# Kernel tuning notes

Hardware: AMD Instinct MI355X
Metric: run time of the kernel (lower is better)

Reference implementation:

```python
import jax, jax.numpy as jnp
import numpy as np

DIN = 4096
DOUT = 12288
NUM_GATES = DOUT // 3
OFFSET = 1
BS = 4096
Z = 1.0

# fixed 3x5 combine matrix from the module
M = jnp.array([[1., 0., 0., 0., 0.],
               [0., 0., 1., 1., -1.],
               [0., 1., 0., -1., 1.]], dtype=jnp.float32)


def _make_connections():
    g = np.arange(NUM_GATES, dtype=np.int64)
    starts = (g * 3 + OFFSET) % DIN
    conn = (starts[:, None] + np.arange(3, dtype=np.int64)[None, :]) % DIN
    return jnp.asarray(conn, dtype=jnp.int32)


def setup_inputs() -> dict:
    key = jax.random.key(0)
    kx, kw = jax.random.split(key)
    x = jax.random.normal(kx, (BS, DIN), dtype=jnp.float32)
    wgts = jax.random.normal(kw, (NUM_GATES, 3, 4), dtype=jnp.float32)
    connections = _make_connections()
    return {"x": x, "wgts": wgts, "connections": connections}


def reference(x, wgts, connections):
    bs = x.shape[0]
    # gather 3 inputs per gate: [bs, G, 3]
    gathered = x[:, connections]
    # append constant z -> [bs, G, 4]
    zcol = jnp.full((bs, NUM_GATES, 1), Z, dtype=x.dtype)
    inp = jnp.concatenate([gathered, zcol], axis=-1)
    # softmax-weighted small matmul (training path): [G,3,4] x [bs,G,4] -> [bs,G,3]
    wp = jax.nn.softmax(wgts, axis=-1)
    s = jnp.einsum('gik,bgk->bgi', wp, inp)
    # elementwise products -> [bs, G, 5]
    v4 = s[..., 0] * s[..., 1]
    v5 = s[..., 0] * s[..., 2]
    feats = jnp.concatenate([s, v4[..., None], v5[..., None]], axis=-1)
    # fixed 3x5 combine: [bs, G, 3]
    signals = jnp.einsum('rk,bgk->bgr', M, feats)
    # strided slice ::3 on last dim (size 3) keeps only index 0 -> [bs, G]
    out = signals[:, :, ::3].reshape(bs, -1)
    return out
```

## Files before the change

kernel.cpp:

```cpp
#include <hip/hip_runtime.h>

#define DIN 4096
#define NG  4096
#define BS  4096
#define RPB 8
#define BT  1024

typedef float v4f __attribute__((ext_vector_type(4)));

__global__ __launch_bounds__(BT, 4) void fredkin_s0_stream(
    const float* __restrict__ x,
    const float* __restrict__ wgts,
    float* __restrict__ out)
{
    const int tid = threadIdx.x;
    const int l   = tid & 63;
    const int g0  = 4 * tid;

    float4 wq[4];
#pragma unroll
    for (int j = 0; j < 4; ++j) {
        float4 r = *reinterpret_cast<const float4*>(wgts + (size_t)(g0 + j) * 12);
        float m  = fmaxf(fmaxf(r.x, r.y), fmaxf(r.z, r.w));
        float e0 = __expf(r.x - m);
        float e1 = __expf(r.y - m);
        float e2 = __expf(r.z - m);
        float e3 = __expf(r.w - m);
        float inv = 1.0f / (e0 + e1 + e2 + e3);
        wq[j] = make_float4(e0 * inv, e1 * inv, e2 * inv, e3 * inv);
    }

    const int brow = blockIdx.x * RPB;
    const float* xb   = x   + (size_t)brow * DIN;
    float*       orow = out + (size_t)brow * NG + g0;

    const int lb = (12 * tid) & (DIN - 1);
    const int i1 = (lb + 4)  & (DIN - 1);
    const int i2 = (lb + 8)  & (DIN - 1);
    const int i3 = (lb + 12) & (DIN - 1);

#pragma unroll
    for (int r = 0; r < RPB; ++r) {
        const float* xr = xb + (size_t)r * DIN;
        float4 f0 = *reinterpret_cast<const float4*>(xr + lb);
        float4 f1 = *reinterpret_cast<const float4*>(xr + i1);
        float4 f2 = *reinterpret_cast<const float4*>(xr + i2);
        float e12 = __shfl_down(f0.x, 1);
        if (l == 63) e12 = xr[i3];
        v4f o;
        o.x = fmaf(wq[0].x, f0.y, fmaf(wq[0].y, f0.z, fmaf(wq[0].z, f0.w, wq[0].w)));
        o.y = fmaf(wq[1].x, f1.x, fmaf(wq[1].y, f1.y, fmaf(wq[1].z, f1.z, wq[1].w)));
        o.z = fmaf(wq[2].x, f1.w, fmaf(wq[2].y, f2.x, fmaf(wq[2].z, f2.y, wq[2].w)));
        o.w = fmaf(wq[3].x, f2.z, fmaf(wq[3].y, f2.w, fmaf(wq[3].z, e12, wq[3].w)));
        __builtin_nontemporal_store(o, reinterpret_cast<v4f*>(orow + (size_t)r * NG));
    }
}

extern "C" void kernel_launch(void* const* d_in, const int* in_sizes, int n_in,
                              void* d_out, int out_size, void* d_ws, size_t ws_size,
                              hipStream_t stream) {
    const float* x    = (const float*)d_in[0];
    const float* wgts = (const float*)d_in[1];
    float* out = (float*)d_out;

    fredkin_s0_stream<<<dim3(BS / RPB), dim3(BT), 0, stream>>>(x, wgts, out);
}
```

Measured before the change: 127.2 us.

## Stage input rows through LDS ring buffer with async global-to-LDS loads

Replaces direct per-thread float4 global loads of x with a 4-buffer LDS ring filled by global_load_lds DMA, prefetching up to three rows ahead, with manual vmcnt waits and a barrier per row. Gates are remapped so each thread handles gates tid+1024k, which gives coalesced scalar output stores in place of per-thread float4 stores, and reads of the gathered inputs come from LDS. The aim is to overlap row loads with compute and stores and to avoid the shuffle and edge-case scalar load. In exchange it adds 16 KB of LDS per block, a barrier on every row, and fragile hand-counted waitcnt values that mix in the store counts.

```diff
diff --git a/kernel.cpp b/kernel.cpp
--- a/kernel.cpp
+++ b/kernel.cpp
@@ -1,59 +1,100 @@
 #include <hip/hip_runtime.h>
 
-#define DIN 4096
-#define NG  4096
-#define BS  4096
-#define RPB 8
-#define BT  1024
+#define DIN  4096
+#define NG   4096
+#define BS   4096
+#define RPB  8
+#define BT   1024
 
-typedef float v4f __attribute__((ext_vector_type(4)));
+#define WAITVM(N) __builtin_amdgcn_s_waitcnt((N) | 0x0F70)
 
-__global__ __launch_bounds__(BT, 4) void fredkin_s0_stream(
+__device__ __forceinline__ void dma16(const float* g, float* lds) {
+    __builtin_amdgcn_global_load_lds(
+        (const __attribute__((address_space(1))) void*)g,
+        (__attribute__((address_space(3))) void*)lds, 16, 0, 0);
+}
+
+__global__ __launch_bounds__(BT, 8) void fredkin_ring4(
     const float* __restrict__ x,
     const float* __restrict__ wgts,
     float* __restrict__ out)
 {
+    __shared__ float B0[DIN], B1[DIN], B2[DIN], B3[DIN];
+
     const int tid = threadIdx.x;
+    const int w   = tid >> 6;
     const int l   = tid & 63;
-    const int g0  = 4 * tid;
 
     float4 wq[4];
 #pragma unroll
-    for (int j = 0; j < 4; ++j) {
-        float4 r = *reinterpret_cast<const float4*>(wgts + (size_t)(g0 + j) * 12);
+    for (int k = 0; k < 4; ++k) {
+        const int g = tid + (k << 10);
+        float4 r = *reinterpret_cast<const float4*>(wgts + (size_t)g * 12);
         float m  = fmaxf(fmaxf(r.x, r.y), fmaxf(r.z, r.w));
         float e0 = __expf(r.x - m);
         float e1 = __expf(r.y - m);
         float e2 = __expf(r.z - m);
         float e3 = __expf(r.w - m);
         float inv = 1.0f / (e0 + e1 + e2 + e3);
-        wq[j] = make_float4(e0 * inv, e1 * inv, e2 * inv, e3 * inv);
+        wq[k] = make_float4(e0 * inv, e1 * inv, e2 * inv, e3 * inv);
     }
 
     const int brow = blockIdx.x * RPB;
     const float* xb   = x   + (size_t)brow * DIN;
-    float*       orow = out + (size_t)brow * NG + g0;
+    float*       obase = out + (size_t)brow * NG + tid;
+    const int doff = (w << 8) + (l << 2);
 
-    const int lb = (12 * tid) & (DIN - 1);
-    const int i1 = (lb + 4)  & (DIN - 1);
-    const int i2 = (lb + 8)  & (DIN - 1);
-    const int i3 = (lb + 12) & (DIN - 1);
+    int idx[4][3];
+#pragma unroll
+    for (int k = 0; k < 4; ++k) {
+        const int jb = 3 * tid + 3072 * k;
+#pragma unroll
+        for (int j = 0; j < 3; ++j) idx[k][j] = (jb + 1 + j) & (DIN - 1);
+    }
 
-#pragma unroll
-    for (int r = 0; r < RPB; ++r) {
-        const float* xr = xb + (size_t)r * DIN;
-        float4 f0 = *reinterpret_cast<const float4*>(xr + lb);
-        float4 f1 = *reinterpret_cast<const float4*>(xr + i1);
-        float4 f2 = *reinterpret_cast<const float4*>(xr + i2);
-        float e12 = __shfl_down(f0.x, 1);
-        if (l == 63) e12 = xr[i3];
-        v4f o;
-        o.x = fmaf(wq[0].x, f0.y, fmaf(wq[0].y, f0.z, fmaf(wq[0].z, f0.w, wq[0].w)));
-        o.y = fmaf(wq[1].x, f1.x, fmaf(wq[1].y, f1.y, fmaf(wq[1].z, f1.z, wq[1].w)));
-        o.z = fmaf(wq[2].x, f1.w, fmaf(wq[2].y, f2.x, fmaf(wq[2].z, f2.y, wq[2].w)));
-        o.w = fmaf(wq[3].x, f2.z, fmaf(wq[3].y, f2.w, fmaf(wq[3].z, e12, wq[3].w)));
-        __builtin_nontemporal_store(o, reinterpret_cast<v4f*>(orow + (size_t)r * NG));
+#define STAGE(BUF, R_) dma16(xb + (size_t)(R_) * DIN + doff, (BUF) + (w << 8));
+
+    asm volatile("" ::: "memory");
+    STAGE(B0, 0)
+    STAGE(B1, 1)
+    STAGE(B2, 2)
+
+#define FRED_ITER(R_, NWAIT, RBUF, WBUF, DO_STAGE)                            \
+    {                                                                         \
+        asm volatile("" ::: "memory");                                        \
+        WAITVM(NWAIT);                               \
+        __builtin_amdgcn_s_barrier();      \
+        asm volatile("" ::: "memory");                                        \
+        if (DO_STAGE) STAGE(WBUF, (R_) + 3)                                   \
+        float* orow = obase + (size_t)(R_) * NG;                              \
+        float o0 = fmaf(wq[0].x, RBUF[idx[0][0]],                             \
+                   fmaf(wq[0].y, RBUF[idx[0][1]],                             \
+                   fmaf(wq[0].z, RBUF[idx[0][2]], wq[0].w)));                 \
+        float o1 = fmaf(wq[1].x, RBUF[idx[1][0]],                             \
+                   fmaf(wq[1].y, RBUF[idx[1][1]],                             \
+                   fmaf(wq[1].z, RBUF[idx[1][2]], wq[1].w)));                 \
+        float o2 = fmaf(wq[2].x, RBUF[idx[2][0]],                             \
+                   fmaf(wq[2].y, RBUF[idx[2][1]],                             \
+                   fmaf(wq[2].z, RBUF[idx[2][2]], wq[2].w)));                 \
+        float o3 = fmaf(wq[3].x, RBUF[idx[3][0]],                             \
+                   fmaf(wq[3].y, RBUF[idx[3][1]],                             \
+                   fmaf(wq[3].z, RBUF[idx[3][2]], wq[3].w)));                 \
+        __builtin_nontemporal_store(o0, orow);                                \
+        __builtin_nontemporal_store(o1, orow + 1024);                         \
+        __builtin_nontemporal_store(o2, orow + 2048);                         \
+        __builtin_nontemporal_store(o3, orow + 3072);                         \
     }
+
+    FRED_ITER(0,  2, B0, B3, 1)
+    FRED_ITER(1,  6, B1, B0, 1)
+    FRED_ITER(2, 10, B2, B1, 1)
+    FRED_ITER(3, 14, B3, B2, 1)
+    FRED_ITER(4, 14, B0, B3, 1)
+    FRED_ITER(5, 14, B1, B0, 0)
+    FRED_ITER(6, 13, B2, B1, 0)
+    FRED_ITER(7, 12, B3, B2, 0)
+#undef FRED_ITER
+#undef STAGE
 }
 
 extern "C" void kernel_launch(void* const* d_in, const int* in_sizes, int n_in,
@@ -63,5 +104,5 @@
     const float* wgts = (const float*)d_in[1];
     float* out = (float*)d_out;
 
-    fredkin_s0_stream<<<dim3(BS / RPB), dim3(BT), 0, stream>>>(x, wgts, out);
+    fredkin_ring4<<<dim3(BS / RPB), dim3(BT), 0, stream>>>(x, wgts, out);
 }
```

After: 115.7 us. 1.1x faster.
